# Kernel tuning notes

Measured on AMD Instinct MI355X. Metric: run time of the kernel, lower is better.

The kernel has to match this reference:

```python
import jax, jax.numpy as jnp
import numpy as np

B, CIN, COUT, WDIM, H, W = 16, 128, 3, 512, 256, 256

def setup_inputs() -> dict:
    key = jax.random.key(0)
    k1, k2, k3, k4, k5 = jax.random.split(key, 5)
    return {
        "x": jax.random.normal(k1, (B, CIN, H, W), dtype=jnp.float32),
        "w": jax.random.normal(k2, (B, WDIM), dtype=jnp.float32),
        "weight": jax.random.normal(k3, (COUT, CIN, 1, 1), dtype=jnp.float32),
        "bias": jnp.zeros((COUT,), dtype=jnp.float32),
        "affine_w": jax.random.normal(k4, (CIN, WDIM), dtype=jnp.float32),
        "affine_b": jax.random.normal(k5, (CIN,), dtype=jnp.float32),
    }

def reference(x, w, weight, bias, affine_w, affine_b):
    # style = affine(w): [B, CIN]
    style = jnp.einsum('bd,cd->bc', w, affine_w) + affine_b
    # per-sample modulated 1x1 conv == scale input channels by style, then GEMM
    wmat = weight[:, :, 0, 0]  # [COUT, CIN]
    xm = x * style[:, :, None, None]  # [B, CIN, H, W]
    out = jnp.einsum('bihw,oi->bohw', xm, wmat) + bias[None, :, None, None]
    return out
```

## Files before the change

### kernel.cpp

```cpp
#include <hip/hip_runtime.h>

#define B_    16
#define CIN_  128
#define COUT_ 3
#define WDIM_ 512
#define HW_   65536

typedef float fvec4 __attribute__((ext_vector_type(4)));

__global__ __launch_bounds__(128) void style_coeff_kernel(
    const float* __restrict__ w,
    const float* __restrict__ weight,
    const float* __restrict__ affine_w,
    const float* __restrict__ affine_b,
    fvec4* __restrict__ coeff)
{
    const int b = blockIdx.x;
    const int c = threadIdx.x;

    const fvec4* wb = (const fvec4*)(w + (size_t)b * WDIM_);
    const fvec4* aw = (const fvec4*)(affine_w + (size_t)c * WDIM_);

    float s = 0.0f;
#pragma unroll 8
    for (int d = 0; d < WDIM_ / 4; ++d) {
        fvec4 a = aw[d];
        fvec4 v = wb[d];
        s += a.x * v.x + a.y * v.y + a.z * v.z + a.w * v.w;
    }
    s += affine_b[c];

    fvec4 o;
    o.x = s * weight[0 * CIN_ + c];
    o.y = s * weight[1 * CIN_ + c];
    o.z = s * weight[2 * CIN_ + c];
    o.w = 0.0f;
    coeff[(size_t)b * CIN_ + c] = o;
}

__global__ __launch_bounds__(256) void torgb_kernel(
    const float*  __restrict__ x,
    const fvec4*  __restrict__ coeff,
    const float*  __restrict__ bias,
    float*        __restrict__ out)
{
    __shared__ fvec4 sc[CIN_];

    const int b = blockIdx.y;
    const int t = threadIdx.x;

    if (t < CIN_) sc[t] = coeff[(size_t)b * CIN_ + t];
    __syncthreads();

    const size_t p4 = ((size_t)blockIdx.x * 256 + t) * 4;
    const float* xb = x + (size_t)b * CIN_ * HW_ + p4;

    fvec4 a0 = {0.f, 0.f, 0.f, 0.f};
    fvec4 a1 = {0.f, 0.f, 0.f, 0.f};
    fvec4 a2 = {0.f, 0.f, 0.f, 0.f};

#pragma unroll 16
    for (int i = 0; i < CIN_; ++i) {
        fvec4 xv = *(const fvec4*)(xb + (size_t)i * HW_);
        fvec4 c  = sc[i];
        a0.x = fmaf(xv.x, c.x, a0.x);
        a0.y = fmaf(xv.y, c.x, a0.y);
        a0.z = fmaf(xv.z, c.x, a0.z);
        a0.w = fmaf(xv.w, c.x, a0.w);
        a1.x = fmaf(xv.x, c.y, a1.x);
        a1.y = fmaf(xv.y, c.y, a1.y);
        a1.z = fmaf(xv.z, c.y, a1.z);
        a1.w = fmaf(xv.w, c.y, a1.w);
        a2.x = fmaf(xv.x, c.z, a2.x);
        a2.y = fmaf(xv.y, c.z, a2.y);
        a2.z = fmaf(xv.z, c.z, a2.z);
        a2.w = fmaf(xv.w, c.z, a2.w);
    }

    const float b0 = bias[0], b1 = bias[1], b2 = bias[2];
    float* ob = out + (size_t)b * COUT_ * HW_ + p4;

    fvec4 r0 = {a0.x + b0, a0.y + b0, a0.z + b0, a0.w + b0};
    fvec4 r1 = {a1.x + b1, a1.y + b1, a1.z + b1, a1.w + b1};
    fvec4 r2 = {a2.x + b2, a2.y + b2, a2.z + b2, a2.w + b2};

    __builtin_nontemporal_store(r0, (fvec4*)(ob + 0 * (size_t)HW_));
    __builtin_nontemporal_store(r1, (fvec4*)(ob + 1 * (size_t)HW_));
    __builtin_nontemporal_store(r2, (fvec4*)(ob + 2 * (size_t)HW_));
}

extern "C" void kernel_launch(void* const* d_in, const int* in_sizes, int n_in,
                              void* d_out, int out_size, void* d_ws, size_t ws_size,
                              hipStream_t stream) {
    const float* x        = (const float*)d_in[0];
    const float* w        = (const float*)d_in[1];
    const float* weight   = (const float*)d_in[2];
    const float* bias     = (const float*)d_in[3];
    const float* affine_w = (const float*)d_in[4];
    const float* affine_b = (const float*)d_in[5];
    float* out = (float*)d_out;

    fvec4* coeff = (fvec4*)d_ws;

    style_coeff_kernel<<<dim3(B_), dim3(CIN_), 0, stream>>>(
        w, weight, affine_w, affine_b, coeff);

    dim3 grid(HW_ / (4 * 256), B_);
    torgb_kernel<<<grid, dim3(256), 0, stream>>>(x, coeff, bias, out);
}
```

Baseline: 700.5 us.

## Process four pixel sweeps per thread with batched channel loads

Each thread now handles four 4-pixel groups spaced 1024 pixels apart and loads four channels of them at once, keeping 12 vector accumulators. The grid shrinks fourfold so each block covers 4096 pixels. The goal is more independent loads in flight per thread to hide memory latency. The cost is fewer blocks and waves per CU and more register pressure.

Result: slower. 715.6 us (+2.2%).

```diff
diff --git a/kernel.cpp b/kernel.cpp
--- a/kernel.cpp
+++ b/kernel.cpp
@@ -5,6 +5,9 @@
 #define COUT_ 3
 #define WDIM_ 512
 #define HW_   65536
+
+#define TILE_PX  4096
+#define SWEEP_PX 1024
 
 typedef float fvec4 __attribute__((ext_vector_type(4)));
 
@@ -52,41 +55,49 @@
     if (t < CIN_) sc[t] = coeff[(size_t)b * CIN_ + t];
     __syncthreads();
 
-    const size_t p4 = ((size_t)blockIdx.x * 256 + t) * 4;
-    const float* xb = x + (size_t)b * CIN_ * HW_ + p4;
+    const size_t p0 = (size_t)blockIdx.x * TILE_PX + (size_t)t * 4;
+    const float* xb = x + (size_t)b * CIN_ * HW_ + p0;
 
-    fvec4 a0 = {0.f, 0.f, 0.f, 0.f};
-    fvec4 a1 = {0.f, 0.f, 0.f, 0.f};
-    fvec4 a2 = {0.f, 0.f, 0.f, 0.f};
+    fvec4 acc[4][3];
+#pragma unroll
+    for (int k = 0; k < 4; ++k)
+#pragma unroll
+        for (int o = 0; o < 3; ++o)
+            acc[k][o] = (fvec4){0.f, 0.f, 0.f, 0.f};
 
-#pragma unroll 16
-    for (int i = 0; i < CIN_; ++i) {
-        fvec4 xv = *(const fvec4*)(xb + (size_t)i * HW_);
-        fvec4 c  = sc[i];
-        a0.x = fmaf(xv.x, c.x, a0.x);
-        a0.y = fmaf(xv.y, c.x, a0.y);
-        a0.z = fmaf(xv.z, c.x, a0.z);
-        a0.w = fmaf(xv.w, c.x, a0.w);
-        a1.x = fmaf(xv.x, c.y, a1.x);
-        a1.y = fmaf(xv.y, c.y, a1.y);
-        a1.z = fmaf(xv.z, c.y, a1.z);
-        a1.w = fmaf(xv.w, c.y, a1.w);
-        a2.x = fmaf(xv.x, c.z, a2.x);
-        a2.y = fmaf(xv.y, c.z, a2.y);
-        a2.z = fmaf(xv.z, c.z, a2.z);
-        a2.w = fmaf(xv.w, c.z, a2.w);
+    for (int i = 0; i < CIN_; i += 4) {
+        fvec4 xv[4][4];
+#pragma unroll
+        for (int di = 0; di < 4; ++di)
+#pragma unroll
+            for (int k = 0; k < 4; ++k)
+                xv[di][k] = *(const fvec4*)(xb + (size_t)(i + di) * HW_
+                                               + (size_t)k * SWEEP_PX);
+
+#pragma unroll
+        for (int di = 0; di < 4; ++di) {
+            const fvec4 c = sc[i + di];
+#pragma unroll
+            for (int k = 0; k < 4; ++k) {
+                acc[k][0] += xv[di][k] * c.x;
+                acc[k][1] += xv[di][k] * c.y;
+                acc[k][2] += xv[di][k] * c.z;
+            }
+        }
     }
 
     const float b0 = bias[0], b1 = bias[1], b2 = bias[2];
-    float* ob = out + (size_t)b * COUT_ * HW_ + p4;
+    float* ob = out + (size_t)b * COUT_ * HW_ + p0;
 
-    fvec4 r0 = {a0.x + b0, a0.y + b0, a0.z + b0, a0.w + b0};
-    fvec4 r1 = {a1.x + b1, a1.y + b1, a1.z + b1, a1.w + b1};
-    fvec4 r2 = {a2.x + b2, a2.y + b2, a2.z + b2, a2.w + b2};
-
-    __builtin_nontemporal_store(r0, (fvec4*)(ob + 0 * (size_t)HW_));
-    __builtin_nontemporal_store(r1, (fvec4*)(ob + 1 * (size_t)HW_));
-    __builtin_nontemporal_store(r2, (fvec4*)(ob + 2 * (size_t)HW_));
+#pragma unroll
+    for (int k = 0; k < 4; ++k) {
+        fvec4 r0 = acc[k][0] + b0;
+        fvec4 r1 = acc[k][1] + b1;
+        fvec4 r2 = acc[k][2] + b2;
+        __builtin_nontemporal_store(r0, (fvec4*)(ob + 0 * (size_t)HW_ + (size_t)k * SWEEP_PX));
+        __builtin_nontemporal_store(r1, (fvec4*)(ob + 1 * (size_t)HW_ + (size_t)k * SWEEP_PX));
+        __builtin_nontemporal_store(r2, (fvec4*)(ob + 2 * (size_t)HW_ + (size_t)k * SWEEP_PX));
+    }
 }
 
 extern "C" void kernel_launch(void* const* d_in, const int* in_sizes, int n_in,
@@ -105,6 +116,6 @@
     style_coeff_kernel<<<dim3(B_), dim3(CIN_), 0, stream>>>(
         w, weight, affine_w, affine_b, coeff);
 
-    dim3 grid(HW_ / (4 * 256), B_);
+    dim3 grid(HW_ / TILE_PX, B_);
     torgb_kernel<<<grid, dim3(256), 0, stream>>>(x, coeff, bias, out);
 }
```
